# Optimization experiments

Measured on AMD Instinct MI355X. Metric: run time of the kernel, lower is better.

## Reference

```python
import jax, jax.numpy as jnp
import numpy as np

B, S, H = 4, 2048, 4096          # batch, seq_len, hidden_size
E, K, T = 64, 4, 4               # entities/sample, concepts/entity, subtokens/entity
NC, D, KI = 100000, 100, 2048    # concept vocab, interlayer dim, kg_intermediate
EPS = 1e-6
NEG = -1e9


def setup_inputs() -> dict:
    key = jax.random.key(0)
    ks = jax.random.split(key, 12)
    inp = {}
    inp["hidden_states"] = jax.random.normal(ks[0], (B, S, H), jnp.float32)
    inp["words_ents"] = jax.random.randint(ks[1], (B, E, K), 0, NC, dtype=jnp.int32)
    # unique subtoken positions per sample (torch index_copy with dup indices is undefined)
    perm = jax.vmap(lambda k: jax.random.permutation(k, S))(jax.random.split(ks[2], B))
    inp["words_subtoken"] = perm[:, : E * T].reshape(B, E, T).astype(jnp.int32)
    inp["concept_embed"] = jax.random.normal(ks[3], (NC, D), jnp.float32) * 0.02
    inp["sentinel"] = jax.random.normal(ks[4], (D,), jnp.float32) * 0.02
    inp["ln_w"] = jnp.ones((H,), jnp.float32)
    inp["gate_w"] = jax.random.normal(ks[5], (D, KI), jnp.float32) * 0.02
    inp["up_w"] = jax.random.normal(ks[6], (D, KI), jnp.float32) * 0.02
    inp["down_w"] = jax.random.normal(ks[7], (KI, H), jnp.float32) * 0.02
    inp["mlp_w"] = jax.random.normal(ks[8], (H + D, H), jnp.float32) * 0.02
    inp["mlp_b"] = jnp.zeros((H,), jnp.float32)
    inp["alpha"] = jnp.full((1,), 0.5, jnp.float32)
    return inp


def _rmsnorm(x, w):
    xf = x.astype(jnp.float32)
    var = jnp.mean(xf * xf, axis=-1, keepdims=True)
    return (w * (xf * jax.lax.rsqrt(var + EPS))).astype(x.dtype)


def reference(hidden_states, words_ents, words_subtoken, concept_embed, sentinel,
              ln_w, gate_w, up_w, down_w, mlp_w, mlp_b, alpha):
    residual = hidden_states
    hs = _rmsnorm(hidden_states, ln_w)                                   # [B,S,H]
    hs_pad = jnp.concatenate([hs, jnp.zeros((B, 1, H), hs.dtype)], 1)    # [B,S+1,H] pad row

    # entity concept embeddings + knowledge sentinel
    ce = jnp.where(words_ents == -1, 0, words_ents)
    ent_ori = jnp.concatenate(
        [concept_embed[ce], jnp.broadcast_to(sentinel, (B, E, 1, D))], axis=2)  # [B,E,K+1,D]
    # KGMLP: down(silu(gate(x)) * up(x)) : D -> H
    conv = (jax.nn.silu(ent_ori @ gate_w) * (ent_ori @ up_w)) @ down_w   # [B,E,K+1,H]

    # mean of subtoken hidden states per entity (pad -1 -> zero pad row)
    wst = jnp.where(words_subtoken == -1, S, words_subtoken)             # [B,E,T]
    cnt = jnp.maximum((words_subtoken != -1).sum(-1), 1).astype(hs.dtype)
    gathered = jax.vmap(lambda h, i: h[i])(hs_pad, wst)                  # [B,E,T,H]
    b = gathered.sum(axis=2) / cnt[..., None]                            # [B,E,H]

    # attention over K concepts + sentinel
    logits = jnp.einsum('bekh,beh->bek', conv, b).astype(jnp.float32)    # [B,E,K+1]
    mask = jnp.where(words_ents == -1, NEG, 0.0).astype(jnp.float32)
    mask = jnp.concatenate([mask, jnp.zeros((B, E, 1), jnp.float32)], -1)
    attn = jax.nn.softmax(logits + mask, axis=-1).astype(ent_ori.dtype)
    attn_out = jnp.einsum('bek,bekd->bed', attn, ent_ori)                # [B,E,D]

    # scatter entity summaries to their subtoken positions
    vals = jnp.broadcast_to(attn_out[:, :, None, :], (B, E, T, D)).reshape(B, E * T, D)
    idx = wst.reshape(B, E * T)
    tmp = jax.vmap(lambda i, v: jnp.zeros((S + 1, D), hs.dtype).at[i].set(v))(idx, vals)

    kg = jnp.concatenate([hs_pad, tmp], axis=-1)[:, :-1]                 # [B,S,H+D]
    out = jax.nn.silu(kg @ mlp_w + mlp_b)                                # [B,S,H]
    return out * alpha + residual
```

## Files before the change

kernel.cpp:

```cpp
#include <hip/hip_runtime.h>
#include <hip/hip_bf16.h>

constexpr int B_ = 4, S_ = 2048, H_ = 4096;
constexpr int E_ = 64, K_ = 4, T_ = 4;
constexpr int D_ = 100, KI_ = 2048;
constexpr float EPS_ = 1e-6f;
constexpr float NEG_ = -1e9f;

typedef _Float16 f16x8 __attribute__((ext_vector_type(8)));
typedef _Float16 f16x4 __attribute__((ext_vector_type(4)));
typedef float    f32x4 __attribute__((ext_vector_type(4)));

#define GLL(gp, ldsbyte)                                                        \
    __builtin_amdgcn_global_load_lds(                                           \
        (__attribute__((address_space(1))) void*)(uintptr_t)(gp),               \
        (__attribute__((address_space(3))) void*)(uintptr_t)((char*)smem + (ldsbyte)), \
        16, 0, 0)

__global__ __launch_bounds__(256) void k_rmsnorm(const float* __restrict__ x,
                                                 const float* __restrict__ w,
                                                 _Float16* __restrict__ a16) {
    const int row = blockIdx.x;
    const int t = threadIdx.x;
    const float4* xr = reinterpret_cast<const float4*>(x + (size_t)row * H_);
    const float4* wr = reinterpret_cast<const float4*>(w);

    float4 v[4];
    float ss = 0.f;
#pragma unroll
    for (int i = 0; i < 4; ++i) {
        v[i] = xr[t + 256 * i];
        ss += v[i].x * v[i].x + v[i].y * v[i].y + v[i].z * v[i].z + v[i].w * v[i].w;
    }
    __shared__ float red[4];
#pragma unroll
    for (int off = 32; off; off >>= 1) ss += __shfl_down(ss, off);
    if ((t & 63) == 0) red[t >> 6] = ss;
    __syncthreads();
    if (t == 0) {
        float s = red[0] + red[1] + red[2] + red[3];
        red[0] = rsqrtf(s / (float)H_ + EPS_);
    }
    __syncthreads();
    const float scale = red[0];
#pragma unroll
    for (int i = 0; i < 4; ++i) {
        float4 wv = wr[t + 256 * i];
        f16x4 hv;
        hv[0] = (_Float16)(v[i].x * scale * wv.x);
        hv[1] = (_Float16)(v[i].y * scale * wv.y);
        hv[2] = (_Float16)(v[i].z * scale * wv.z);
        hv[3] = (_Float16)(v[i].w * scale * wv.w);
        *reinterpret_cast<f16x4*>(a16 + (size_t)row * H_ + 4 * (t + 256 * i)) = hv;
    }
}

__global__ __launch_bounds__(256) void k_wsplit(const float* __restrict__ w1,
                                                _Float16* __restrict__ bt16) {
    __shared__ float sT[64][68];
    const int k0 = blockIdx.x * 64;
    const int n0 = blockIdx.y * 64;
    const int t = threadIdx.x;

#pragma unroll
    for (int q = 0; q < 4; ++q) {
        const int r = (t >> 4) + q * 16;
        const int c = (t & 15) * 4;
        float4 v = *reinterpret_cast<const float4*>(&w1[(size_t)(k0 + r) * H_ + n0 + c]);
        *reinterpret_cast<float4*>(&sT[r][c]) = v;
    }
    __syncthreads();
#pragma unroll
    for (int p = 0; p < 2; ++p) {
        const int n = (t >> 3) + p * 32;
        const int kc = (t & 7) * 8;
        f16x8 hv;
#pragma unroll
        for (int j = 0; j < 8; ++j) hv[j] = (_Float16)sT[kc + j][n];
        *reinterpret_cast<f16x8*>(bt16 + (size_t)(n0 + n) * H_ + k0 + kc) = hv;
    }
}

__global__ __launch_bounds__(256) void k_entori(const int* __restrict__ we,
                                                const float* __restrict__ cemb,
                                                const float* __restrict__ sent,
                                                float* __restrict__ ent,
                                                int* __restrict__ inv) {
    const int be = blockIdx.x;
    const int t = threadIdx.x;
    if (t < 32) inv[be * 32 + t] = -1;
    for (int idx = t; idx < 5 * D_; idx += 256) {
        const int k = idx / D_, d = idx % D_;
        float v;
        if (k < K_) {
            int c = we[be * K_ + k];
            if (c < 0) c = 0;
            v = cemb[(size_t)c * D_ + d];
        } else {
            v = sent[d];
        }
        ent[(size_t)be * (5 * D_) + idx] = v;
    }
}

__global__ __launch_bounds__(256) void k_invset(const int* __restrict__ wst,
                                                int* __restrict__ inv) {
    const int be = threadIdx.x;
    if (be < B_ * E_) {
        const int b = be / E_;
#pragma unroll
        for (int j = 0; j < T_; ++j) {
            int p = wst[be * T_ + j];
            if (p >= 0 && p < S_) inv[b * S_ + p] = be;
        }
    }
}

__global__ __launch_bounds__(256) void k_bvec(const _Float16* __restrict__ a16,
                                              const int* __restrict__ wst,
                                              float* __restrict__ bvec) {
    const int be = blockIdx.x;
    const int b = be / E_;
    const int t = threadIdx.x;

    int pos[T_];
    int cnt = 0;
#pragma unroll
    for (int j = 0; j < T_; ++j) {
        int p = wst[be * T_ + j];
        if (p >= 0) cnt++; else p = -1;
        pos[j] = p;
    }
    const float inv = 1.f / (float)(cnt > 0 ? cnt : 1);

    float acc[16] = {};
#pragma unroll
    for (int j = 0; j < T_; ++j) {
        if (pos[j] >= 0) {
            const f16x8* rh = reinterpret_cast<const f16x8*>(
                a16 + ((size_t)b * S_ + pos[j]) * H_ + t * 16);
#pragma unroll
            for (int c2 = 0; c2 < 2; ++c2) {
                f16x8 h = rh[c2];
#pragma unroll
                for (int e = 0; e < 8; ++e) acc[c2 * 8 + e] += (float)h[e];
            }
        }
    }
    float4* dst = reinterpret_cast<float4*>(bvec + (size_t)be * H_ + t * 16);
#pragma unroll
    for (int c = 0; c < 4; ++c) {
        float4 r = {acc[4 * c] * inv, acc[4 * c + 1] * inv,
                    acc[4 * c + 2] * inv, acc[4 * c + 3] * inv};
        dst[c] = r;
    }
}

__global__ __launch_bounds__(256) void k_gateup(const float* __restrict__ ent,
                                                const float* __restrict__ gw,
                                                const float* __restrict__ uw,
                                                float* __restrict__ h1) {
    __shared__ float sA[64][D_];
    __shared__ float sG[D_][64];
    const int n0 = blockIdx.x * 64;
    const int m0 = blockIdx.y * 64;
    const int t = threadIdx.x;
    const int tx = t & 15, ty = t >> 4;

    for (int idx = t; idx < 64 * D_; idx += 256) {
        int m = idx / D_, d = idx % D_;
        sA[m][d] = ent[(size_t)(m0 + m) * D_ + d];
    }
    for (int idx = t; idx < D_ * 64; idx += 256) {
        int d = idx / 64, n = idx % 64;
        sG[d][n] = gw[(size_t)d * KI_ + n0 + n];
    }
    __syncthreads();

    float g[4][4] = {}, u[4][4] = {};
    for (int d = 0; d < D_; ++d) {
        float a[4], bg[4];
        float4 bu = *reinterpret_cast<const float4*>(&uw[(size_t)d * KI_ + n0 + tx * 4]);
        float bub[4] = {bu.x, bu.y, bu.z, bu.w};
#pragma unroll
        for (int i = 0; i < 4; ++i) a[i] = sA[ty * 4 + i][d];
#pragma unroll
        for (int j = 0; j < 4; ++j) bg[j] = sG[d][tx * 4 + j];
#pragma unroll
        for (int i = 0; i < 4; ++i)
#pragma unroll
            for (int j = 0; j < 4; ++j) {
                g[i][j] += a[i] * bg[j];
                u[i][j] += a[i] * bub[j];
            }
    }
#pragma unroll
    for (int i = 0; i < 4; ++i) {
        float4 r;
        float* rv = &r.x;
#pragma unroll
        for (int j = 0; j < 4; ++j) {
            float gv = g[i][j];
            rv[j] = (gv / (1.f + expf(-gv))) * u[i][j];
        }
        *reinterpret_cast<float4*>(&h1[(size_t)(m0 + ty * 4 + i) * KI_ + n0 + tx * 4]) = r;
    }
}

__global__ __launch_bounds__(256) void k_bd(const float* __restrict__ bvec,
                                            const float* __restrict__ dw,
                                            float* __restrict__ bdp) {
    __shared__ float sA[64][20];
    __shared__ float sB[64][20];
    const int n0 = blockIdx.x * 64;
    const int m0 = blockIdx.y * 64;
    const int z = blockIdx.z;
    const int t = threadIdx.x;
    const int tx = t & 15, ty = t >> 4;
    const int lr = t >> 2, lc = (t & 3) * 4;

    float acc[4][4] = {};
    for (int k0 = z * 512; k0 < (z + 1) * 512; k0 += 16) {
        *reinterpret_cast<float4*>(&sA[lr][lc]) =
            *reinterpret_cast<const float4*>(&bvec[(size_t)(m0 + lr) * H_ + k0 + lc]);
        *reinterpret_cast<float4*>(&sB[lr][lc]) =
            *reinterpret_cast<const float4*>(&dw[(size_t)(n0 + lr) * H_ + k0 + lc]);
        __syncthreads();
#pragma unroll
        for (int kk = 0; kk < 16; ++kk) {
            float a[4], b[4];
#pragma unroll
            for (int i = 0; i < 4; ++i) a[i] = sA[ty * 4 + i][kk];
#pragma unroll
            for (int j = 0; j < 4; ++j) b[j] = sB[tx * 4 + j][kk];
#pragma unroll
            for (int i = 0; i < 4; ++i)
#pragma unroll
                for (int j = 0; j < 4; ++j) acc[i][j] += a[i] * b[j];
        }
        __syncthreads();
    }
#pragma unroll
    for (int i = 0; i < 4; ++i) {
        float4 r = {acc[i][0], acc[i][1], acc[i][2], acc[i][3]};
        *reinterpret_cast<float4*>(
            &bdp[((size_t)z * 256 + m0 + ty * 4 + i) * KI_ + n0 + tx * 4]) = r;
    }
}

__global__ __launch_bounds__(256) void k_attn(const float* __restrict__ h1,
                                              const float* __restrict__ bdp,
                                              const float* __restrict__ ent,
                                              const int* __restrict__ we,
                                              float* __restrict__ attn_out) {
    __shared__ float sbd[KI_];
    __shared__ float red[4];
    __shared__ float sl[8];
    const int be = blockIdx.x;
    const int t = threadIdx.x;

    for (int i = t; i < KI_; i += 256) {
        float s = 0.f;
#pragma unroll
        for (int z = 0; z < 8; ++z) s += bdp[((size_t)z * 256 + be) * KI_ + i];
        sbd[i] = s;
    }
    __syncthreads();

    for (int k = 0; k < 5; ++k) {
        const float* hrow = h1 + ((size_t)be * 5 + k) * KI_;
        float s = 0.f;
        for (int i = t; i < KI_; i += 256) s += hrow[i] * sbd[i];
#pragma unroll
        for (int off = 32; off; off >>= 1) s += __shfl_down(s, off);
        if ((t & 63) == 0) red[t >> 6] = s;
        __syncthreads();
        if (t == 0) sl[k] = red[0] + red[1] + red[2] + red[3];
        __syncthreads();
    }
    if (t == 0) {
        float lg[5];
#pragma unroll
        for (int k = 0; k < K_; ++k)
            lg[k] = sl[k] + (we[be * K_ + k] == -1 ? NEG_ : 0.f);
        lg[4] = sl[4];
        float mx = lg[0];
#pragma unroll
        for (int k = 1; k < 5; ++k) mx = fmaxf(mx, lg[k]);
        float sum = 0.f;
#pragma unroll
        for (int k = 0; k < 5; ++k) { lg[k] = expf(lg[k] - mx); sum += lg[k]; }
        float is = 1.f / sum;
#pragma unroll
        for (int k = 0; k < 5; ++k) sl[k] = lg[k] * is;
    }
    __syncthreads();
    if (t < D_) {
        float a = 0.f;
#pragma unroll
        for (int k = 0; k < 5; ++k) a += sl[k] * ent[((size_t)be * 5 + k) * D_ + t];
        attn_out[(size_t)be * D_ + t] = a;
    }
}

__global__ __launch_bounds__(256) void k_entw2(const float* __restrict__ attn_out,
                                               const float* __restrict__ mlpw,
                                               float* __restrict__ entw2) {
    __shared__ float sa[D_];
    const int be = blockIdx.x;
    const int t = threadIdx.x;
    if (t < D_) sa[t] = attn_out[(size_t)be * D_ + t];
    __syncthreads();

    const float* W2 = mlpw + (size_t)H_ * H_;
#pragma unroll
    for (int i = 0; i < 4; ++i) {
        const int h4 = t + 256 * i;
        float4 c = make_float4(0.f, 0.f, 0.f, 0.f);
        for (int d = 0; d < D_; ++d) {
            float4 w = *reinterpret_cast<const float4*>(&W2[(size_t)d * H_ + 4 * h4]);
            float av = sa[d];
            c.x += av * w.x; c.y += av * w.y; c.z += av * w.z; c.w += av * w.w;
        }
        *reinterpret_cast<float4*>(&entw2[(size_t)be * H_ + 4 * h4]) = c;
    }
}

__global__ __launch_bounds__(256) void k_mfma_gemm(const _Float16* __restrict__ A,
                                                   const _Float16* __restrict__ Bt,
                                                   const float* __restrict__ bias,
                                                   const float* __restrict__ resid,
                                                   const float* __restrict__ alphap,
                                                   const float* __restrict__ entw2,
                                                   const int* __restrict__ inv,
                                                   float* __restrict__ Out) {
    __shared__ __align__(16) _Float16 smem[8192];
    const int t = threadIdx.x;
    const int lane = t & 63, wid = t >> 6;
    const int wr = wid >> 1, wc = wid & 1;

    const int bid = blockIdx.x;
    const int swz = (bid & 7) * 256 + (bid >> 3);
    const int mb = swz >> 5, nb = swz & 31;
    const size_t m0 = (size_t)mb * 128, n0 = (size_t)nb * 128;

    const int c0 = wid * 128 + lane, c1 = c0 + 64;
    const size_t offA0 = ((size_t)(m0 + (c0 >> 2))) * H_ + (c0 & 3) * 8;
    const size_t offA1 = ((size_t)(m0 + (c1 >> 2))) * H_ + (c1 & 3) * 8;
    const size_t offB0 = ((size_t)(n0 + (c0 >> 2))) * H_ + (c0 & 3) * 8;
    const size_t offB1 = ((size_t)(n0 + (c1 >> 2))) * H_ + (c1 & 3) * 8;
    const unsigned ldsW = wid * 2048;

    const int fr = lane & 15;
    const int kq = (lane >> 4) * 8;

    f32x4 acc[4][4] = {};

    for (int k0 = 0; k0 < H_; k0 += 32) {
        GLL(A + offA0 + k0, ldsW);
        GLL(A + offA1 + k0, ldsW + 1024);
        GLL(Bt + offB0 + k0, 8192 + ldsW);
        GLL(Bt + offB1 + k0, 8192 + ldsW + 1024);
        __syncthreads();

        f16x8 af[4], bf[4];
#pragma unroll
        for (int i = 0; i < 4; ++i) {
            af[i] = *reinterpret_cast<const f16x8*>(smem + (wr * 64 + i * 16 + fr) * 32 + kq);
            bf[i] = *reinterpret_cast<const f16x8*>(smem + 4096 + (wc * 64 + i * 16 + fr) * 32 + kq);
        }
#pragma unroll
        for (int i = 0; i < 4; ++i)
#pragma unroll
            for (int j = 0; j < 4; ++j)
                acc[i][j] = __builtin_amdgcn_mfma_f32_16x16x32_f16(af[i], bf[j], acc[i][j], 0, 0, 0);
        __syncthreads();
    }

    const float alpha = alphap[0];
    const int cr = (lane >> 4) * 4;
    const int cc = lane & 15;
#pragma unroll
    for (int i = 0; i < 4; ++i) {
        const int rowbase = (int)m0 + wr * 64 + i * 16 + cr;
        int bes[4];
#pragma unroll
        for (int r = 0; r < 4; ++r) bes[r] = inv[rowbase + r];
#pragma unroll
        for (int j = 0; j < 4; ++j) {
            const int col = (int)n0 + wc * 64 + j * 16 + cc;
            const float bv = bias[col];
#pragma unroll
            for (int r = 0; r < 4; ++r) {
                float v = acc[i][j][r] + bv;
                if (bes[r] >= 0) v += entw2[(size_t)bes[r] * H_ + col];
                const size_t o = (size_t)(rowbase + r) * H_ + col;
                Out[o] = (v / (1.f + expf(-v))) * alpha + resid[o];
            }
        }
    }
}

extern "C" void kernel_launch(void* const* d_in, const int* in_sizes, int n_in,
                              void* d_out, int out_size, void* d_ws, size_t ws_size,
                              hipStream_t stream) {
    const float* hidden = (const float*)d_in[0];
    const int*   we     = (const int*)d_in[1];
    const int*   wst    = (const int*)d_in[2];
    const float* cemb   = (const float*)d_in[3];
    const float* sent   = (const float*)d_in[4];
    const float* lnw    = (const float*)d_in[5];
    const float* gw     = (const float*)d_in[6];
    const float* uw     = (const float*)d_in[7];
    const float* dw     = (const float*)d_in[8];
    const float* mlpw   = (const float*)d_in[9];
    const float* mlpb   = (const float*)d_in[10];
    const float* alpha  = (const float*)d_in[11];
    float* out = (float*)d_out;

    char* w = (char*)d_ws;
    _Float16* a16   = (_Float16*)(w);
    _Float16* bt16  = (_Float16*)(w + 67108864);
    float*    bvec  = (float*)(w + 100663296);
    float*    ent   = (float*)(w + 104857600);
    float*    h1    = (float*)(w + 105369600);
    float*    bdp   = (float*)(w + 115855360);
    float*    attn  = (float*)(w + 132632576);
    float*    entw2 = (float*)(w + 132734976);
    int*      inv   = (int*)(w + 136929280);

    k_rmsnorm<<<B_ * S_, 256, 0, stream>>>(hidden, lnw, a16);
    k_wsplit<<<dim3(H_ / 64, H_ / 64), 256, 0, stream>>>(mlpw, bt16);
    k_entori<<<B_ * E_, 256, 0, stream>>>(we, cemb, sent, ent, inv);
    k_invset<<<1, 256, 0, stream>>>(wst, inv);
    k_bvec<<<B_ * E_, 256, 0, stream>>>(a16, wst, bvec);
    k_gateup<<<dim3(KI_ / 64, (B_ * E_ * 5) / 64), 256, 0, stream>>>(ent, gw, uw, h1);
    k_bd<<<dim3(KI_ / 64, (B_ * E_) / 64, 8), 256, 0, stream>>>(bvec, dw, bdp);
    k_attn<<<B_ * E_, 256, 0, stream>>>(h1, bdp, ent, we, attn);
    k_entw2<<<B_ * E_, 256, 0, stream>>>(attn, mlpw, entw2);
    k_mfma_gemm<<<(H_ / 128) * ((B_ * S_) / 128), 256, 0, stream>>>(
        a16, bt16, mlpb, hidden, alpha, entw2, inv, out);
}
```

Baseline: 1.060 ms.

## Widen MFMA GEMM K-tile to 64 with XOR-swizzled LDS, interleave small GEMM columns

Result: faster. 986.0 us (-7.0%).

```diff
diff --git a/kernel.cpp b/kernel.cpp
--- a/kernel.cpp
+++ b/kernel.cpp
@@ -179,13 +179,14 @@
 
     float g[4][4] = {}, u[4][4] = {};
     for (int d = 0; d < D_; ++d) {
-        float a[4], bg[4];
-        float4 bu = *reinterpret_cast<const float4*>(&uw[(size_t)d * KI_ + n0 + tx * 4]);
-        float bub[4] = {bu.x, bu.y, bu.z, bu.w};
+        float a[4], bg[4], bub[4];
 #pragma unroll
         for (int i = 0; i < 4; ++i) a[i] = sA[ty * 4 + i][d];
 #pragma unroll
-        for (int j = 0; j < 4; ++j) bg[j] = sG[d][tx * 4 + j];
+        for (int j = 0; j < 4; ++j) {
+            bg[j] = sG[d][tx + 16 * j];
+            bub[j] = uw[(size_t)d * KI_ + n0 + tx + 16 * j];
+        }
 #pragma unroll
         for (int i = 0; i < 4; ++i)
 #pragma unroll
@@ -195,16 +196,13 @@
             }
     }
 #pragma unroll
-    for (int i = 0; i < 4; ++i) {
-        float4 r;
-        float* rv = &r.x;
+    for (int i = 0; i < 4; ++i)
 #pragma unroll
         for (int j = 0; j < 4; ++j) {
             float gv = g[i][j];
-            rv[j] = (gv / (1.f + expf(-gv))) * u[i][j];
-        }
-        *reinterpret_cast<float4*>(&h1[(size_t)(m0 + ty * 4 + i) * KI_ + n0 + tx * 4]) = r;
-    }
+            h1[(size_t)(m0 + ty * 4 + i) * KI_ + n0 + tx + 16 * j] =
+                (gv / (1.f + expf(-gv))) * u[i][j];
+        }
 }
 
 __global__ __launch_bounds__(256) void k_bd(const float* __restrict__ bvec,
@@ -232,7 +230,7 @@
 #pragma unroll
             for (int i = 0; i < 4; ++i) a[i] = sA[ty * 4 + i][kk];
 #pragma unroll
-            for (int j = 0; j < 4; ++j) b[j] = sB[tx * 4 + j][kk];
+            for (int j = 0; j < 4; ++j) b[j] = sB[tx + 16 * j][kk];
 #pragma unroll
             for (int i = 0; i < 4; ++i)
 #pragma unroll
@@ -241,11 +239,10 @@
         __syncthreads();
     }
 #pragma unroll
-    for (int i = 0; i < 4; ++i) {
-        float4 r = {acc[i][0], acc[i][1], acc[i][2], acc[i][3]};
-        *reinterpret_cast<float4*>(
-            &bdp[((size_t)z * 256 + m0 + ty * 4 + i) * KI_ + n0 + tx * 4]) = r;
-    }
+    for (int i = 0; i < 4; ++i)
+#pragma unroll
+        for (int j = 0; j < 4; ++j)
+            bdp[((size_t)z * 256 + m0 + ty * 4 + i) * KI_ + n0 + tx + 16 * j] = acc[i][j];
 }
 
 __global__ __launch_bounds__(256) void k_attn(const float* __restrict__ h1,
@@ -334,7 +331,7 @@
                                                    const float* __restrict__ entw2,
                                                    const int* __restrict__ inv,
                                                    float* __restrict__ Out) {
-    __shared__ __align__(16) _Float16 smem[8192];
+    __shared__ __align__(16) _Float16 smem[16384];
     const int t = threadIdx.x;
     const int lane = t & 63, wid = t >> 6;
     const int wr = wid >> 1, wc = wid & 1;
@@ -344,36 +341,46 @@
     const int mb = swz >> 5, nb = swz & 31;
     const size_t m0 = (size_t)mb * 128, n0 = (size_t)nb * 128;
 
-    const int c0 = wid * 128 + lane, c1 = c0 + 64;
-    const size_t offA0 = ((size_t)(m0 + (c0 >> 2))) * H_ + (c0 & 3) * 8;
-    const size_t offA1 = ((size_t)(m0 + (c1 >> 2))) * H_ + (c1 & 3) * 8;
-    const size_t offB0 = ((size_t)(n0 + (c0 >> 2))) * H_ + (c0 & 3) * 8;
-    const size_t offB1 = ((size_t)(n0 + (c1 >> 2))) * H_ + (c1 & 3) * 8;
-    const unsigned ldsW = wid * 2048;
+    int rowE[4], qE[4];
+#pragma unroll
+    for (int e = 0; e < 4; ++e) {
+        const int c = wid * 256 + e * 64 + lane;
+        rowE[e] = c >> 3;
+        qE[e] = (c & 7) ^ (rowE[e] & 7);
+    }
+    const unsigned ldsA = wid * 4096;
+    const unsigned ldsB = 16384 + wid * 4096;
 
     const int fr = lane & 15;
-    const int kq = (lane >> 4) * 8;
+    const int dq = lane >> 4;
 
     f32x4 acc[4][4] = {};
 
-    for (int k0 = 0; k0 < H_; k0 += 32) {
-        GLL(A + offA0 + k0, ldsW);
-        GLL(A + offA1 + k0, ldsW + 1024);
-        GLL(Bt + offB0 + k0, 8192 + ldsW);
-        GLL(Bt + offB1 + k0, 8192 + ldsW + 1024);
-        __syncthreads();
-
-        f16x8 af[4], bf[4];
-#pragma unroll
-        for (int i = 0; i < 4; ++i) {
-            af[i] = *reinterpret_cast<const f16x8*>(smem + (wr * 64 + i * 16 + fr) * 32 + kq);
-            bf[i] = *reinterpret_cast<const f16x8*>(smem + 4096 + (wc * 64 + i * 16 + fr) * 32 + kq);
-        }
-#pragma unroll
-        for (int i = 0; i < 4; ++i)
-#pragma unroll
-            for (int j = 0; j < 4; ++j)
-                acc[i][j] = __builtin_amdgcn_mfma_f32_16x16x32_f16(af[i], bf[j], acc[i][j], 0, 0, 0);
+    for (int k0 = 0; k0 < H_; k0 += 64) {
+#pragma unroll
+        for (int e = 0; e < 4; ++e) {
+            GLL(A  + (size_t)(m0 + rowE[e]) * H_ + k0 + qE[e] * 8, ldsA + e * 1024);
+            GLL(Bt + (size_t)(n0 + rowE[e]) * H_ + k0 + qE[e] * 8, ldsB + e * 1024);
+        }
+        __syncthreads();
+
+#pragma unroll
+        for (int h = 0; h < 2; ++h) {
+            f16x8 af[4], bf[4];
+            const int slot8 = ((h * 4 + dq) ^ (fr & 7)) * 8;
+#pragma unroll
+            for (int i = 0; i < 4; ++i) {
+                const int ra = wr * 64 + i * 16 + fr;
+                const int rb = wc * 64 + i * 16 + fr;
+                af[i] = *reinterpret_cast<const f16x8*>(smem + ra * 64 + slot8);
+                bf[i] = *reinterpret_cast<const f16x8*>(smem + 8192 + rb * 64 + slot8);
+            }
+#pragma unroll
+            for (int i = 0; i < 4; ++i)
+#pragma unroll
+                for (int j = 0; j < 4; ++j)
+                    acc[i][j] = __builtin_amdgcn_mfma_f32_16x16x32_f16(af[i], bf[j], acc[i][j], 0, 0, 0);
+        }
         __syncthreads();
     }
 
```
